# Performance work log

Measured on AMD Instinct MI355X. Metric: run time of the kernel, lower is better.

Reference implementation:

```python
import jax, jax.numpy as jnp
import numpy as np

N = 50000      # nodes
E = 400000     # edges
DIM = 3        # pseudo-coordinate dim
M = 3          # kernel size per dim (closed B-spline, degree 1)
K = M ** DIM   # 27 basis weights
IN = 32
MID = 32
OUT = 32
EPS = 1e-5


def spline_basis(edge_attr):
    """Degree-1 closed B-spline basis. edge_attr: [E, DIM] in [0,1].
    Returns basis [E, 2^DIM], weight indices [E, 2^DIM] into K."""
    bits = (jnp.arange(2 ** DIM)[:, None] >> jnp.arange(DIM)[None, :]) & 1  # [8, DIM]
    scaled = edge_attr * M                       # closed spline: scale by kernel size
    lo = jnp.floor(scaled)
    frac = scaled - lo                           # [E, DIM]
    b = jnp.where(bits[None].astype(bool), frac[:, None, :], 1.0 - frac[:, None, :])
    basis = jnp.prod(b, axis=-1)                 # [E, 8]
    idx = (lo.astype(jnp.int32)[:, None, :] + bits[None]) % M  # [E, 8, DIM]
    strides = M ** jnp.arange(DIM)               # [1, 3, 9]
    widx = jnp.sum(idx * strides, axis=-1)       # [E, 8] in [0, K)
    return basis, widx


def spline_conv(x, src, dst, basis, widx, W, root, bias):
    """x: [N, in]; W: [K, in, out]; mean aggregation + root weight + bias."""
    x_j = x[src]                                          # gather [E, in]
    upd = basis[:, :, None] * x_j[:, None, :]             # [E, 8, in]
    # scatter-add basis-weighted source features into per-(node, weight-idx) bins
    S = jnp.zeros((N, K, x.shape[1]), x.dtype).at[dst[:, None], widx].add(upd)
    deg = jnp.zeros((N,), x.dtype).at[dst].add(1.0)
    deg = jnp.maximum(deg, 1.0)
    msg = jnp.einsum('nki,kio->no', S, W) / deg[:, None]  # mean over incoming edges
    return msg + x @ root + bias


def batchnorm(h, gamma, beta):
    mu = jnp.mean(h, axis=0)
    var = jnp.var(h, axis=0)  # biased, as in torch BN forward
    return (h - mu) * jax.lax.rsqrt(var + EPS) * gamma + beta


def setup_inputs() -> dict:
    key = jax.random.key(0)
    ks = jax.random.split(key, 16)
    d = {}
    d['x'] = jax.random.normal(ks[0], (N, IN), jnp.float32)
    d['edge_index'] = jax.random.randint(ks[1], (2, E), 0, N, dtype=jnp.int32)
    d['edge_attr'] = jax.random.uniform(ks[2], (E, DIM), dtype=jnp.float32)
    d['pos'] = jax.random.normal(ks[3], (N, DIM), jnp.float32)
    def wscale(fan_in):
        return 1.0 / np.sqrt(fan_in)
    d['W1'] = jax.random.normal(ks[4], (K, IN, MID), jnp.float32) * wscale(IN)
    d['root1'] = jax.random.normal(ks[5], (IN, MID), jnp.float32) * wscale(IN)
    d['b1'] = jnp.zeros((MID,), jnp.float32)
    d['W2'] = jax.random.normal(ks[6], (K, MID, 2 * MID), jnp.float32) * wscale(MID)
    d['root2'] = jax.random.normal(ks[7], (MID, 2 * MID), jnp.float32) * wscale(MID)
    d['b2'] = jnp.zeros((2 * MID,), jnp.float32)
    d['gamma'] = jnp.ones((2 * MID,), jnp.float32)
    d['beta'] = jnp.zeros((2 * MID,), jnp.float32)
    c3_in = 2 * MID + 3
    d['W3'] = jax.random.normal(ks[8], (K, c3_in, OUT), jnp.float32) * wscale(c3_in)
    d['root3'] = jax.random.normal(ks[9], (c3_in, OUT), jnp.float32) * wscale(c3_in)
    d['b3'] = jnp.zeros((OUT,), jnp.float32)
    return d


def reference(x, edge_index, edge_attr, pos, W1, root1, b1, W2, root2, b2,
              gamma, beta, W3, root3, b3):
    src, dst = edge_index[0], edge_index[1]
    basis, widx = spline_basis(edge_attr)
    h = jax.nn.elu(spline_conv(x, src, dst, basis, widx, W1, root1, b1))
    h = jax.nn.elu(batchnorm(spline_conv(h, src, dst, basis, widx, W2, root2, b2), gamma, beta))
    h = jnp.concatenate([h, pos], axis=1)
    out = spline_conv(h, src, dst, basis, widx, W3, root3, b3)
    return out
```

## Files before the change

kernel.cpp:

```cpp
#include <hip/hip_runtime.h>
#include <hip/hip_bf16.h>


#define EPS 1e-5f
#define MAXN 50176
#define MAXE 401408
#define SP2 904

typedef __attribute__((ext_vector_type(8))) short short8;
typedef __attribute__((ext_vector_type(4))) float floatx4;

__device__ int             g_deg[MAXN];
__device__ int             g_offs[MAXN + 1];
__device__ int             g_cursor[MAXN];
__device__ int             g_bsum[256];
__device__ uint4           g_emeta[MAXE * 2];
__device__ __align__(16) __hip_bfloat16 g_h0[MAXN * 32];
__device__ __align__(16) __hip_bfloat16 g_h1[MAXN * 32];
__device__ __align__(16) __hip_bfloat16 g_h2[MAXN * 64];
__device__ __align__(16) __hip_bfloat16 g_h3[MAXN * 96];
__device__ __align__(16) __hip_bfloat16 g_Z[(size_t)MAXN * 896];
__device__ __align__(16) __hip_bfloat16 g_Wp1[28672];
__device__ __align__(16) __hip_bfloat16 g_Wp2[57344];
__device__ __align__(16) __hip_bfloat16 g_Wp3[86016];
__device__ float           g_stats[128];
__device__ int             g_isbf16;

__device__ __forceinline__ float loadf(const void* p, int i, bool bf)
{
    return bf ? (float)((const __hip_bfloat16*)p)[i] : ((const float*)p)[i];
}
__device__ __forceinline__ float bf16f(unsigned int u)
{
    return __uint_as_float(u << 16);
}
__device__ __forceinline__ unsigned short bfbits(float f)
{
    union { __hip_bfloat16 h; unsigned short u; } cv;
    cv.h = __float2bfloat16(f);
    return cv.u;
}

__global__ void init_detect(const unsigned int* __restrict__ x, int n)
{
    int i = blockIdx.x * blockDim.x + threadIdx.x;
    if (blockIdx.x == 0 && threadIdx.x < 64) {
        int lane = threadIdx.x;
        int cnt = 0;
        for (int k = lane; k < 256; k += 64) {
            unsigned int lo = x[k] & 0xFFFFu;
            int ex = (int)((lo >> 7) & 0xFFu);
            if (lo == 0u || (ex >= 96 && ex <= 140)) cnt++;
        }
#pragma unroll
        for (int o = 1; o < 64; o <<= 1) cnt += __shfl_xor(cnt, o, 64);
        if (lane == 0) g_isbf16 = (cnt >= 200) ? 1 : 0;
    }
    if (i < n) { g_deg[i] = 0; g_cursor[i] = 0; }
    if (i < 128) g_stats[i] = 0.0f;
}

template <int COUT>
__device__ __forceinline__ void prep_ws_dev(const void* W, const void* root,
                                            __hip_bfloat16* Wp, int t, bool bf)
{
    int j = t & 7;
    int lane = (t >> 3) & 63;
    int rest = t >> 9;
    int kk = rest % 28;
    int nt = rest / 28;
    int k = kk * 32 + (lane >> 4) * 8 + j;
    int o = nt * 16 + (lane & 15);
    float v = (k < 864) ? loadf(W, k * COUT + o, bf)
                        : loadf(root, (k - 864) * COUT + o, bf);
    Wp[t] = __float2bfloat16(v);
}

__device__ __forceinline__ void prep_w3_dev(const void* W, const void* root,
                                            __hip_bfloat16* Wp, int t, bool bf)
{
    const int KB = 3;
    int j = t & 7;
    int lane = (t >> 3) & 63;
    int rest = t >> 9;
    int kk = rest % KB;
    int nt = rest / KB;
    int k = kk * 32 + (lane >> 4) * 8 + j;
    int ncol = nt * 16 + (lane & 15);
    int kw = ncol >> 5;
    int o = ncol & 31;
    float v = 0.0f;
    if (k < 67)
        v = (kw < 27) ? loadf(W, (kw * 67 + k) * 32 + o, bf)
                      : loadf(root, k * 32 + o, bf);
    Wp[t] = __float2bfloat16(v);
}

__global__ void misc_kernel(const int* __restrict__ dst, const void* __restrict__ x,
                            const void* W1, const void* r1,
                            const void* W2, const void* r2,
                            const void* W3, const void* r3, int E, int N)
{
    int t = blockIdx.x * blockDim.x + threadIdx.x;
    const bool bf = (g_isbf16 != 0);
    if (t < E) { atomicAdd(&g_deg[dst[t]], 1); return; }
    t -= E;
    int nx = N * 32;
    if (t < nx) { g_h0[t] = __float2bfloat16(loadf(x, t, bf)); return; }
    t -= nx;
    if (t < 28672) { prep_ws_dev<32>(W1, r1, g_Wp1, t, bf); return; }
    t -= 28672;
    if (t < 57344) { prep_ws_dev<64>(W2, r2, g_Wp2, t, bf); return; }
    t -= 57344;
    if (t < 86016) { prep_w3_dev(W3, r3, g_Wp3, t, bf); return; }
}

__global__ void scan_blk(int n)
{
    __shared__ int buf[256];
    int tid = threadIdx.x;
    int i = blockIdx.x * 256 + tid;
    int v = (i < n) ? g_deg[i] : 0;
    buf[tid] = v;
    __syncthreads();
    for (int o = 1; o < 256; o <<= 1) {
        int t = (tid >= o) ? buf[tid - o] : 0;
        __syncthreads();
        buf[tid] += t;
        __syncthreads();
    }
    if (i < n) g_offs[i] = buf[tid] - v;
    if (tid == 255) g_bsum[blockIdx.x] = buf[255];
}

__global__ void scan_top(int nb, int n)
{
    __shared__ int buf[256];
    int tid = threadIdx.x;
    int v = (tid < nb) ? g_bsum[tid] : 0;
    buf[tid] = v;
    __syncthreads();
    for (int o = 1; o < 256; o <<= 1) {
        int t = (tid >= o) ? buf[tid - o] : 0;
        __syncthreads();
        buf[tid] += t;
        __syncthreads();
    }
    if (tid < nb) g_bsum[tid] = buf[tid] - v;
    if (tid == nb - 1) g_offs[n] = buf[tid];
}

__global__ void scan_add(int n)
{
    int i = blockIdx.x * 256 + threadIdx.x;
    if (i < n) g_offs[i] += g_bsum[i >> 8];
}

__global__ void basis_fill(const void* __restrict__ attr,
                           const int* __restrict__ src,
                           const int* __restrict__ dst, int E)
{
    int e = blockIdx.x * blockDim.x + threadIdx.x;
    if (e >= E) return;
    const bool bf = (g_isbf16 != 0);
    float f[3];
    int lo[3];
#pragma unroll
    for (int d = 0; d < 3; ++d) {
        float a = loadf(attr, e * 3 + d, bf);
        float s = a * 3.0f;
        float l = floorf(s);
        lo[d] = (int)l;
        f[d] = s - l;
    }
    const int p3[3] = {1, 3, 9};
    unsigned int wxp0 = 0, wxp1 = 0;
    unsigned short bb[8];
#pragma unroll
    for (int b = 0; b < 8; ++b) {
        float w = 1.0f;
        int id = 0;
#pragma unroll
        for (int d = 0; d < 3; ++d) {
            int bit = (b >> d) & 1;
            w *= bit ? f[d] : (1.0f - f[d]);
            id += ((lo[d] + bit) % 3) * p3[d];
        }
        if (b < 4) wxp0 |= (unsigned int)id << (8 * b);
        else       wxp1 |= (unsigned int)id << (8 * (b - 4));
        bb[b] = bfbits(w);
    }
    int d = dst[e];
    int p = atomicAdd(&g_cursor[d], 1);
    int slot = g_offs[d] + p;
    g_emeta[slot * 2] = make_uint4(wxp0, wxp1,
                                   (unsigned int)bb[0] | ((unsigned int)bb[1] << 16),
                                   (unsigned int)bb[2] | ((unsigned int)bb[3] << 16));
    g_emeta[slot * 2 + 1] = make_uint4(
        (unsigned int)bb[4] | ((unsigned int)bb[5] << 16),
        (unsigned int)bb[6] | ((unsigned int)bb[7] << 16),
        (unsigned int)src[e], 0u);
}

template <int COUT, bool ELU, int IN_SEL, int OUT_SEL>
__global__ __launch_bounds__(512, 8) void fused_conv(const void* __restrict__ bias,
                                                     int N)
{
    __shared__ unsigned short Sb[8 * SP2];
    __shared__ uint4 recs[8][64];
    __shared__ float invd[8];
    int tid = threadIdx.x, wid = tid >> 6, lane = tid & 63;
    int nbase = blockIdx.x * 8;
    const bool bf = (g_isbf16 != 0);
    const unsigned short* xptr = (IN_SEL == 0) ? (const unsigned short*)g_h0
                                               : (const unsigned short*)g_h1;
    const __hip_bfloat16* Wp = (COUT == 32) ? g_Wp1 : g_Wp2;

    int n = nbase + wid;
    int m = lane & 15, quad = lane >> 4;

    if (n < N) {
        int e0 = g_offs[n], e1 = g_offs[n + 1];
        floatx4 C00 = {}, C01 = {}, C10 = {}, C11 = {};
        uint4* myrec = &recs[wid][0];
        int bin0 = m, bin1 = m + 16;
        for (int base = e0; base < e1; base += 32) {
            int cnt = e1 - base; if (cnt > 32) cnt = 32;
            if (lane < 32) {
                uint4 v0 = make_uint4(0, 0, 0, 0), v1 = make_uint4(0, 0, 0, 0);
                if (lane < cnt) {
                    size_t le = (size_t)(base + lane) * 2;
                    v0 = g_emeta[le];
                    v1 = g_emeta[le + 1];
                }
                myrec[2 * lane] = v0;
                myrec[2 * lane + 1] = v1;
            }
            __builtin_amdgcn_s_waitcnt(0);
            int jmax = (cnt + 3) >> 2;
            unsigned a0w[4] = {0, 0, 0, 0}, a1w[4] = {0, 0, 0, 0};
            unsigned b0w[4] = {0, 0, 0, 0}, b1w[4] = {0, 0, 0, 0};
#pragma unroll
            for (int j = 0; j < 8; ++j) {
                if (j >= jmax) break;
                int kidx = j * 4 + quad;
                uint4 ra = myrec[2 * kidx];
                uint2 rb = *(const uint2*)&myrec[2 * kidx + 1];
                int sn = (int)((const unsigned*)&myrec[2 * kidx + 1])[2];
                unsigned av0 = xptr[(size_t)sn * 32 + m];
                unsigned av1 = xptr[(size_t)sn * 32 + 16 + m];
                unsigned p0 = 0, p1 = 0;
#pragma unroll
                for (int b = 0; b < 8; ++b) {
                    unsigned wx = ((b < 4 ? ra.x : ra.y) >> (8 * (b & 3))) & 0xFFu;
                    unsigned basw = (b < 2) ? ra.z : (b < 4) ? ra.w
                                  : (b < 6) ? rb.x : rb.y;
                    unsigned bas = (b & 1) ? (basw >> 16) : (basw & 0xFFFFu);
                    if (wx == (unsigned)bin0) p0 = bas;
                    if (wx == (unsigned)bin1) p1 = bas;
                }
                unsigned sh = 16 * (j & 1);
                a0w[j >> 1] |= av0 << sh;
                a1w[j >> 1] |= av1 << sh;
                b0w[j >> 1] |= p0 << sh;
                b1w[j >> 1] |= p1 << sh;
            }
            union U { unsigned w[4]; short8 v; } A0, A1, B0, B1;
#pragma unroll
            for (int q = 0; q < 4; ++q) {
                A0.w[q] = a0w[q]; A1.w[q] = a1w[q];
                B0.w[q] = b0w[q]; B1.w[q] = b1w[q];
            }
            C00 = __builtin_amdgcn_mfma_f32_16x16x32_bf16(A0.v, B0.v, C00, 0, 0, 0);
            C01 = __builtin_amdgcn_mfma_f32_16x16x32_bf16(A0.v, B1.v, C01, 0, 0, 0);
            C10 = __builtin_amdgcn_mfma_f32_16x16x32_bf16(A1.v, B0.v, C10, 0, 0, 0);
            C11 = __builtin_amdgcn_mfma_f32_16x16x32_bf16(A1.v, B1.v, C11, 0, 0, 0);
        }
        unsigned short* Srow = Sb + wid * SP2;
        {
            floatx4 Cf[4] = {C00, C01, C10, C11};
#pragma unroll
            for (int f = 0; f < 4; ++f) {
                int mt = f >> 1, nt = f & 1;
                int bin = nt * 16 + m;
                if (bin < 27) {
                    union { unsigned short h[4]; uint2 u; } pk;
#pragma unroll
                    for (int r = 0; r < 4; ++r) pk.h[r] = bfbits(Cf[f][r]);
                    *(uint2*)(Srow + bin * 32 + mt * 16 + quad * 4) = pk.u;
                }
            }
        }
        if (lane < 32) Srow[864 + lane] = xptr[(size_t)n * 32 + lane];
        if (lane == 0) {
            int deg = e1 - e0;
            invd[wid] = 1.0f / (float)(deg < 1 ? 1 : deg);
        }
    }
    __syncthreads();

    if (wid * 16 < COUT) {
        int mrow = m & 7;
        const unsigned short* Ab = Sb + mrow * SP2 + quad * 8;
        floatx4 accS = {}, accR = {};
#pragma unroll
        for (int kk = 0; kk < 28; ++kk) {
            short8 a = *(const short8*)(Ab + kk * 32);
            const short* bp = (const short*)Wp +
                ((size_t)(wid * 28 + kk) * 64 + lane) * 8;
            short8 b = *(const short8*)bp;
            if (kk < 27) accS = __builtin_amdgcn_mfma_f32_16x16x32_bf16(a, b, accS, 0, 0, 0);
            else         accR = __builtin_amdgcn_mfma_f32_16x16x32_bf16(a, b, accR, 0, 0, 0);
        }
        int o = wid * 16 + m;
        float bval = loadf(bias, o, bf);
#pragma unroll
        for (int r = 0; r < 4; ++r) {
            int slot = quad * 4 + r;
            if (slot >= 8) continue;
            int nn = nbase + slot;
            if (nn >= N) continue;
            float v = accS[r] * invd[slot] + accR[r] + bval;
            if (ELU) v = v > 0.0f ? v : expm1f(v);
            if (OUT_SEL == 1) g_h1[nn * 32 + o] = __float2bfloat16(v);
            else              g_h2[nn * 64 + o] = __float2bfloat16(v);
        }
    }
}

__global__ void bn_reduce(int n)
{
    int tid = threadIdx.x;
    int c = tid & 63;
    int r = tid >> 6;
    float s = 0.0f, s2 = 0.0f;
    for (int i = blockIdx.x * 4 + r; i < n; i += gridDim.x * 4) {
        float v = (float)g_h2[i * 64 + c];
        s += v; s2 += v * v;
    }
    __shared__ float b1s[256], b2s[256];
    b1s[tid] = s; b2s[tid] = s2;
    __syncthreads();
    if (r == 0) {
        s  = b1s[c] + b1s[c + 64] + b1s[c + 128] + b1s[c + 192];
        s2 = b2s[c] + b2s[c + 64] + b2s[c + 128] + b2s[c + 192];
        atomicAdd(&g_stats[c], s);
        atomicAdd(&g_stats[64 + c], s2);
    }
}

__global__ void h3_build(const void* __restrict__ pos,
                         const void* __restrict__ gamma,
                         const void* __restrict__ beta, int N)
{
    __shared__ float cf[128];
    int t = threadIdx.x;
    const bool bf = (g_isbf16 != 0);
    if (t < 64) {
        float inv_n = 1.0f / (float)N;
        float mu = g_stats[t] * inv_n;
        float var = g_stats[64 + t] * inv_n - mu * mu;
        float A = rsqrtf(var + EPS) * loadf(gamma, t, bf);
        cf[t] = A;
        cf[64 + t] = loadf(beta, t, bf) - mu * A;
    }
    __syncthreads();
    int idx = blockIdx.x * blockDim.x + t;
    if (idx >= N * 96) return;
    int n = idx / 96, ch = idx - n * 96;
    float v;
    if (ch < 64) {
        float h = (float)g_h2[n * 64 + ch];
        v = h * cf[ch] + cf[64 + ch];
        v = v > 0.0f ? v : expm1f(v);
    } else if (ch < 67) {
        v = loadf(pos, n * 3 + (ch - 64), bf);
    } else {
        v = 0.0f;
    }
    g_h3[(size_t)n * 96 + ch] = __float2bfloat16(v);
}

template <int STRIDE, int NTOT, int KPAD, int NPW>
__global__ __launch_bounds__(256) void gemm_kernel(int MT, int NTW)
{
    int gid = blockIdx.x * 256 + threadIdx.x;
    int gw = gid >> 6, lane = gid & 63;
    if (gw >= MT * NTW) return;
    int mt = gw / NTW;
    int ntb = (gw % NTW) * NPW;
    int m = lane & 15, quad = lane >> 4;
    const short* hrow = (const short*)g_h3 + (size_t)(mt * 16 + m) * STRIDE;
    floatx4 acc[NPW] = {};
    const int KB = KPAD / 32;
#pragma unroll
    for (int kk = 0; kk < KB; ++kk) {
        short8 a = *(const short8*)(hrow + kk * 32 + quad * 8);
#pragma unroll
        for (int i = 0; i < NPW; ++i) {
            const short* bp = (const short*)g_Wp3 +
                (((size_t)(ntb + i) * KB + kk) * 64 + lane) * 8;
            short8 b = *(const short8*)bp;
            acc[i] = __builtin_amdgcn_mfma_f32_16x16x32_bf16(a, b, acc[i], 0, 0, 0);
        }
    }
    int col = lane & 15;
    int rowbase = mt * 16 + quad * 4;
#pragma unroll
    for (int i = 0; i < NPW; ++i) {
        int ncol = (ntb + i) * 16 + col;
#pragma unroll
        for (int r = 0; r < 4; ++r)
            g_Z[(size_t)(rowbase + r) * NTOT + ncol] = __float2bfloat16(acc[i][r]);
    }
}

template <int COUT, int NTOT>
__global__ __launch_bounds__(256) void agg_kernel(const void* __restrict__ bias,
                                                  void* __restrict__ out_ext, int N)
{
    int wid = threadIdx.x >> 6, lane = threadIdx.x & 63;
    int n = blockIdx.x * 4 + wid;
    if (n >= N) return;
    const bool bf = (g_isbf16 != 0);
    const unsigned short* zp = (const unsigned short*)g_Z;
    int e0 = g_offs[n], e1 = g_offs[n + 1];
    float acc = 0.0f;
    int o = lane & 31, bh = lane >> 5;
    for (int base = e0; base < e1; base += 32) {
        int cnt = e1 - base; if (cnt > 32) cnt = 32;
        uint4 r0 = make_uint4(0, 0, 0, 0), r1 = make_uint4(0, 0, 0, 0);
        if ((lane & 31) < cnt) {
            size_t le = (size_t)(base + (lane & 31)) * 2;
            r0 = g_emeta[le];
            r1 = g_emeta[le + 1];
        }
        int selw4 = (int)(bh ? r0.y : r0.x);
        int selba = (int)(bh ? r1.x : r0.z);
        int selbb = (int)(bh ? r1.y : r0.w);
        int srcv  = (int)r1.z;
#pragma unroll 2
        for (int j = 0; j < cnt; ++j) {
            int sl = j + (bh << 5);
            int sn = __shfl(srcv, j, 64);
            unsigned int w4  = (unsigned int)__shfl(selw4, sl, 64);
            unsigned int ba  = (unsigned int)__shfl(selba, sl, 64);
            unsigned int bbv = (unsigned int)__shfl(selbb, sl, 64);
            const unsigned short* zr = zp + (size_t)sn * NTOT;
#pragma unroll
            for (int bi = 0; bi < 4; ++bi) {
                int wxv = (int)((w4 >> (8 * bi)) & 0xFFu);
                unsigned int bbits = (((bi & 2) ? bbv : ba) >> (16 * (bi & 1))) & 0xFFFFu;
                acc += bf16f(bbits) * bf16f(zr[wxv * 32 + o]);
            }
        }
    }
    acc += __shfl_xor(acc, 32, 64);
    if (lane >= 32) return;
    int deg = e1 - e0;
    float inv = 1.0f / (float)(deg < 1 ? 1 : deg);
    float v = acc * inv + bf16f(zp[(size_t)n * NTOT + 27 * COUT + o])
            + loadf(bias, o, bf);
    if (bf) ((__hip_bfloat16*)out_ext)[n * COUT + o] = __float2bfloat16(v);
    else    ((float*)out_ext)[n * COUT + o] = v;
}

extern "C" void kernel_launch(void* const* d_in, const int* in_sizes, int n_in,
                              void* d_out, int out_size, void* d_ws, size_t ws_size,
                              hipStream_t stream)
{
    const void* x      = d_in[0];
    const int*  eindex = (const int*)d_in[1];
    const void* eattr  = d_in[2];
    const void* pos    = d_in[3];
    const void* W1     = d_in[4];
    const void* root1  = d_in[5];
    const void* b1     = d_in[6];
    const void* W2     = d_in[7];
    const void* root2  = d_in[8];
    const void* b2     = d_in[9];
    const void* gamma  = d_in[10];
    const void* beta   = d_in[11];
    const void* W3     = d_in[12];
    const void* root3  = d_in[13];
    const void* b3     = d_in[14];
    (void)d_ws; (void)ws_size; (void)n_in; (void)out_size;

    const int N = in_sizes[0] / 32;
    const int E = in_sizes[1] / 2;
    const int* srcp = eindex;
    const int* dstp = eindex + E;

    init_detect<<<(N + 255) / 256, 256, 0, stream>>>((const unsigned int*)x, N);
    {
        int tot = E + N * 32 + 28672 + 57344 + 86016;
        misc_kernel<<<(tot + 255) / 256, 256, 0, stream>>>(
            dstp, x, W1, root1, W2, root2, W3, root3, E, N);
    }
    int nb = (N + 255) / 256;
    scan_blk<<<nb, 256, 0, stream>>>(N);
    scan_top<<<1, 256, 0, stream>>>(nb, N);
    scan_add<<<nb, 256, 0, stream>>>(N);
    basis_fill<<<(E + 255) / 256, 256, 0, stream>>>(eattr, srcp, dstp, E);

    int nb8 = (N + 7) / 8;
    fused_conv<32, true, 0, 1><<<nb8, 512, 0, stream>>>(b1, N);
    fused_conv<64, false, 1, 2><<<nb8, 512, 0, stream>>>(b2, N);
    bn_reduce<<<120, 256, 0, stream>>>(N);
    h3_build<<<(N * 96 + 255) / 256, 256, 0, stream>>>(pos, gamma, beta, N);
    {
        const int NTOT = 28 * 32, KPAD = 96, NPW = 4;
        int NTW = (NTOT / 16) / NPW;
        int MT = (N + 15) / 16;
        int waves = MT * NTW;
        gemm_kernel<96, NTOT, KPAD, NPW><<<(waves + 3) / 4, 256, 0, stream>>>(MT, NTW);
    }
    agg_kernel<32, 28 * 32><<<(N + 3) / 4, 256, 0, stream>>>(b3, d_out, N);
}
```

Measured before the change: 365.5 us.

## Fuse layer-3 spline conv into aggregate-then-transform kernel, dropping Z buffer

Replaces the transform-then-gather path for layer 3 (a GEMM writing a per-node 896-wide Z buffer, then an edge-gather kernel) with one fused kernel. For each node it builds the per-bin aggregated features S in LDS using MFMA, then multiplies by the repacked W3/root weights, reduces the split-K partials and writes the output. This removes roughly 90MB of Z writes and the random gathers of Z rows, at the cost of more MFMA work per node (K=2688), higher LDS usage and lower occupancy.

```diff
diff --git a/kernel.cpp b/kernel.cpp
--- a/kernel.cpp
+++ b/kernel.cpp
@@ -6,6 +6,7 @@
 #define MAXN 50176
 #define MAXE 401408
 #define SP2 904
+#define SP3 2696
 
 typedef __attribute__((ext_vector_type(8))) short short8;
 typedef __attribute__((ext_vector_type(4))) float floatx4;
@@ -19,7 +20,6 @@
 __device__ __align__(16) __hip_bfloat16 g_h1[MAXN * 32];
 __device__ __align__(16) __hip_bfloat16 g_h2[MAXN * 64];
 __device__ __align__(16) __hip_bfloat16 g_h3[MAXN * 96];
-__device__ __align__(16) __hip_bfloat16 g_Z[(size_t)MAXN * 896];
 __device__ __align__(16) __hip_bfloat16 g_Wp1[28672];
 __device__ __align__(16) __hip_bfloat16 g_Wp2[57344];
 __device__ __align__(16) __hip_bfloat16 g_Wp3[86016];
@@ -79,20 +79,23 @@
 __device__ __forceinline__ void prep_w3_dev(const void* W, const void* root,
                                             __hip_bfloat16* Wp, int t, bool bf)
 {
-    const int KB = 3;
+    const int KB = 84;
     int j = t & 7;
     int lane = (t >> 3) & 63;
     int rest = t >> 9;
     int kk = rest % KB;
     int nt = rest / KB;
     int k = kk * 32 + (lane >> 4) * 8 + j;
-    int ncol = nt * 16 + (lane & 15);
-    int kw = ncol >> 5;
-    int o = ncol & 31;
+    int o = nt * 16 + (lane & 15);
     float v = 0.0f;
-    if (k < 67)
-        v = (kw < 27) ? loadf(W, (kw * 67 + k) * 32 + o, bf)
-                      : loadf(root, k * 32 + o, bf);
+    if (k < 2592) {
+        int bin = k / 96;
+        int ch = k - bin * 96;
+        if (ch < 67) v = loadf(W, (bin * 67 + ch) * 32 + o, bf);
+    } else {
+        int ch = k - 2592;
+        if (ch < 67) v = loadf(root, ch * 32 + o, bf);
+    }
     Wp[t] = __float2bfloat16(v);
 }
 
@@ -328,6 +331,156 @@
     }
 }
 
+__global__ __launch_bounds__(512, 4) void fused_conv3(const void* __restrict__ bias,
+                                                      void* __restrict__ out_ext,
+                                                      int N)
+{
+    __shared__ __align__(16) unsigned short Sb[8 * SP3];
+    __shared__ union {
+        uint4 recs[8][64];
+        float red[6][64][4];
+    } u;
+    __shared__ float invd[8];
+    int tid = threadIdx.x, wid = tid >> 6, lane = tid & 63;
+    int nbase = blockIdx.x * 8;
+    const bool bf = (g_isbf16 != 0);
+    const unsigned short* xptr = (const unsigned short*)g_h3;
+
+    int n = nbase + wid;
+    int m = lane & 15, quad = lane >> 4;
+
+    if (n < N) {
+        int e0 = g_offs[n], e1 = g_offs[n + 1];
+        floatx4 C[6][2];
+#pragma unroll
+        for (int t = 0; t < 6; ++t) {
+            C[t][0] = (floatx4){0.f, 0.f, 0.f, 0.f};
+            C[t][1] = (floatx4){0.f, 0.f, 0.f, 0.f};
+        }
+        uint4* myrec = &u.recs[wid][0];
+        int bin0 = m, bin1 = m + 16;
+        for (int base = e0; base < e1; base += 32) {
+            int cnt = e1 - base; if (cnt > 32) cnt = 32;
+            if (lane < 32) {
+                uint4 v0 = make_uint4(0, 0, 0, 0), v1 = make_uint4(0, 0, 0, 0);
+                if (lane < cnt) {
+                    size_t le = (size_t)(base + lane) * 2;
+                    v0 = g_emeta[le];
+                    v1 = g_emeta[le + 1];
+                }
+                myrec[2 * lane] = v0;
+                myrec[2 * lane + 1] = v1;
+            }
+            __builtin_amdgcn_s_waitcnt(0);
+            int jmax = (cnt + 3) >> 2;
+            unsigned aw[6][4] = {{0, 0, 0, 0}, {0, 0, 0, 0}, {0, 0, 0, 0},
+                                 {0, 0, 0, 0}, {0, 0, 0, 0}, {0, 0, 0, 0}};
+            unsigned b0w[4] = {0, 0, 0, 0}, b1w[4] = {0, 0, 0, 0};
+#pragma unroll
+            for (int j = 0; j < 8; ++j) {
+                if (j >= jmax) break;
+                int kidx = j * 4 + quad;
+                uint4 ra = myrec[2 * kidx];
+                uint2 rb = *(const uint2*)&myrec[2 * kidx + 1];
+                int sn = (int)((const unsigned*)&myrec[2 * kidx + 1])[2];
+                const unsigned short* hr = xptr + (size_t)sn * 96 + m;
+                unsigned av[6];
+#pragma unroll
+                for (int t = 0; t < 6; ++t) av[t] = hr[t * 16];
+                unsigned p0 = 0, p1 = 0;
+#pragma unroll
+                for (int b = 0; b < 8; ++b) {
+                    unsigned wx = ((b < 4 ? ra.x : ra.y) >> (8 * (b & 3))) & 0xFFu;
+                    unsigned basw = (b < 2) ? ra.z : (b < 4) ? ra.w
+                                  : (b < 6) ? rb.x : rb.y;
+                    unsigned bas = (b & 1) ? (basw >> 16) : (basw & 0xFFFFu);
+                    if (wx == (unsigned)bin0) p0 = bas;
+                    if (wx == (unsigned)bin1) p1 = bas;
+                }
+                unsigned sh = 16 * (j & 1);
+#pragma unroll
+                for (int t = 0; t < 6; ++t) aw[t][j >> 1] |= av[t] << sh;
+                b0w[j >> 1] |= p0 << sh;
+                b1w[j >> 1] |= p1 << sh;
+            }
+            union U { unsigned w[4]; short8 v; } A, B0, B1;
+#pragma unroll
+            for (int q = 0; q < 4; ++q) { B0.w[q] = b0w[q]; B1.w[q] = b1w[q]; }
+#pragma unroll
+            for (int t = 0; t < 6; ++t) {
+#pragma unroll
+                for (int q = 0; q < 4; ++q) A.w[q] = aw[t][q];
+                C[t][0] = __builtin_amdgcn_mfma_f32_16x16x32_bf16(A.v, B0.v, C[t][0], 0, 0, 0);
+                C[t][1] = __builtin_amdgcn_mfma_f32_16x16x32_bf16(A.v, B1.v, C[t][1], 0, 0, 0);
+            }
+        }
+        unsigned short* Srow = Sb + wid * SP3;
+#pragma unroll
+        for (int t = 0; t < 6; ++t) {
+#pragma unroll
+            for (int ntile = 0; ntile < 2; ++ntile) {
+                int bin = ntile * 16 + m;
+                if (bin < 27) {
+                    union { unsigned short h[4]; uint2 uu; } pk;
+#pragma unroll
+                    for (int r = 0; r < 4; ++r) pk.h[r] = bfbits(C[t][ntile][r]);
+                    *(uint2*)(Srow + bin * 96 + t * 16 + quad * 4) = pk.uu;
+                }
+            }
+        }
+        for (int t2 = lane; t2 < 96; t2 += 64)
+            Srow[2592 + t2] = xptr[(size_t)n * 96 + t2];
+        if (lane == 0) {
+            int deg = e1 - e0;
+            invd[wid] = 1.0f / (float)(deg < 1 ? 1 : deg);
+        }
+    }
+    __syncthreads();
+
+    int nt = wid & 1, kq = wid >> 1;
+    int mrow = m & 7;
+    const unsigned short* Ab = Sb + mrow * SP3 + quad * 8;
+    floatx4 accS = {}, accR = {};
+    {
+        int kbeg = kq * 21, kend = kbeg + 21;
+        int ksplit = (kend < 81) ? kend : 81;
+        for (int kk = kbeg; kk < ksplit; ++kk) {
+            short8 a = *(const short8*)(Ab + kk * 32);
+            const short* bp = (const short*)g_Wp3 +
+                ((size_t)(nt * 84 + kk) * 64 + lane) * 8;
+            short8 b = *(const short8*)bp;
+            accS = __builtin_amdgcn_mfma_f32_16x16x32_bf16(a, b, accS, 0, 0, 0);
+        }
+        for (int kk = ksplit; kk < kend; ++kk) {
+            short8 a = *(const short8*)(Ab + kk * 32);
+            const short* bp = (const short*)g_Wp3 +
+                ((size_t)(nt * 84 + kk) * 64 + lane) * 8;
+            short8 b = *(const short8*)bp;
+            accR = __builtin_amdgcn_mfma_f32_16x16x32_bf16(a, b, accR, 0, 0, 0);
+        }
+    }
+    if (kq < 3)
+        *(floatx4*)&u.red[wid][lane][0] = accS;
+    __syncthreads();
+    if (kq == 3) {
+#pragma unroll
+        for (int w = 0; w < 3; ++w)
+            accS += *(const floatx4*)&u.red[2 * w + nt][lane][0];
+        int o = nt * 16 + m;
+        float bval = loadf(bias, o, bf);
+#pragma unroll
+        for (int r = 0; r < 4; ++r) {
+            int slot = quad * 4 + r;
+            if (slot >= 8) continue;
+            int nn = nbase + slot;
+            if (nn >= N) continue;
+            float v = accS[r] * invd[slot] + accR[r] + bval;
+            if (bf) ((__hip_bfloat16*)out_ext)[nn * 32 + o] = __float2bfloat16(v);
+            else    ((float*)out_ext)[nn * 32 + o] = v;
+        }
+    }
+}
+
 __global__ void bn_reduce(int n)
 {
     int tid = threadIdx.x;
@@ -379,90 +532,6 @@
         v = 0.0f;
     }
     g_h3[(size_t)n * 96 + ch] = __float2bfloat16(v);
-}
-
-template <int STRIDE, int NTOT, int KPAD, int NPW>
-__global__ __launch_bounds__(256) void gemm_kernel(int MT, int NTW)
-{
-    int gid = blockIdx.x * 256 + threadIdx.x;
-    int gw = gid >> 6, lane = gid & 63;
-    if (gw >= MT * NTW) return;
-    int mt = gw / NTW;
-    int ntb = (gw % NTW) * NPW;
-    int m = lane & 15, quad = lane >> 4;
-    const short* hrow = (const short*)g_h3 + (size_t)(mt * 16 + m) * STRIDE;
-    floatx4 acc[NPW] = {};
-    const int KB = KPAD / 32;
-#pragma unroll
-    for (int kk = 0; kk < KB; ++kk) {
-        short8 a = *(const short8*)(hrow + kk * 32 + quad * 8);
-#pragma unroll
-        for (int i = 0; i < NPW; ++i) {
-            const short* bp = (const short*)g_Wp3 +
-                (((size_t)(ntb + i) * KB + kk) * 64 + lane) * 8;
-            short8 b = *(const short8*)bp;
-            acc[i] = __builtin_amdgcn_mfma_f32_16x16x32_bf16(a, b, acc[i], 0, 0, 0);
-        }
-    }
-    int col = lane & 15;
-    int rowbase = mt * 16 + quad * 4;
-#pragma unroll
-    for (int i = 0; i < NPW; ++i) {
-        int ncol = (ntb + i) * 16 + col;
-#pragma unroll
-        for (int r = 0; r < 4; ++r)
-            g_Z[(size_t)(rowbase + r) * NTOT + ncol] = __float2bfloat16(acc[i][r]);
-    }
-}
-
-template <int COUT, int NTOT>
-__global__ __launch_bounds__(256) void agg_kernel(const void* __restrict__ bias,
-                                                  void* __restrict__ out_ext, int N)
-{
-    int wid = threadIdx.x >> 6, lane = threadIdx.x & 63;
-    int n = blockIdx.x * 4 + wid;
-    if (n >= N) return;
-    const bool bf = (g_isbf16 != 0);
-    const unsigned short* zp = (const unsigned short*)g_Z;
-    int e0 = g_offs[n], e1 = g_offs[n + 1];
-    float acc = 0.0f;
-    int o = lane & 31, bh = lane >> 5;
-    for (int base = e0; base < e1; base += 32) {
-        int cnt = e1 - base; if (cnt > 32) cnt = 32;
-        uint4 r0 = make_uint4(0, 0, 0, 0), r1 = make_uint4(0, 0, 0, 0);
-        if ((lane & 31) < cnt) {
-            size_t le = (size_t)(base + (lane & 31)) * 2;
-            r0 = g_emeta[le];
-            r1 = g_emeta[le + 1];
-        }
-        int selw4 = (int)(bh ? r0.y : r0.x);
-        int selba = (int)(bh ? r1.x : r0.z);
-        int selbb = (int)(bh ? r1.y : r0.w);
-        int srcv  = (int)r1.z;
-#pragma unroll 2
-        for (int j = 0; j < cnt; ++j) {
-            int sl = j + (bh << 5);
-            int sn = __shfl(srcv, j, 64);
-            unsigned int w4  = (unsigned int)__shfl(selw4, sl, 64);
-            unsigned int ba  = (unsigned int)__shfl(selba, sl, 64);
-            unsigned int bbv = (unsigned int)__shfl(selbb, sl, 64);
-            const unsigned short* zr = zp + (size_t)sn * NTOT;
-#pragma unroll
-            for (int bi = 0; bi < 4; ++bi) {
-                int wxv = (int)((w4 >> (8 * bi)) & 0xFFu);
-                unsigned int bbits = (((bi & 2) ? bbv : ba) >> (16 * (bi & 1))) & 0xFFFFu;
-                acc += bf16f(bbits) * bf16f(zr[wxv * 32 + o]);
-            }
-        }
-    }
-    acc += __shfl_xor(acc, 32, 64);
-    if (lane >= 32) return;
-    int deg = e1 - e0;
-    float inv = 1.0f / (float)(deg < 1 ? 1 : deg);
-    float v = acc * inv + bf16f(zp[(size_t)n * NTOT + 27 * COUT + o])
-            + loadf(bias, o, bf);
-    if (bf) ((__hip_bfloat16*)out_ext)[n * COUT + o] = __float2bfloat16(v);
-    else    ((float*)out_ext)[n * COUT + o] = v;
 }
 
 extern "C" void kernel_launch(void* const* d_in, const int* in_sizes, int n_in,
@@ -508,12 +577,5 @@
     fused_conv<64, false, 1, 2><<<nb8, 512, 0, stream>>>(b2, N);
     bn_reduce<<<120, 256, 0, stream>>>(N);
     h3_build<<<(N * 96 + 255) / 256, 256, 0, stream>>>(pos, gamma, beta, N);
-    {
-        const int NTOT = 28 * 32, KPAD = 96, NPW = 4;
-        int NTW = (NTOT / 16) / NPW;
-        int MT = (N + 15) / 16;
-        int waves = MT * NTW;
-        gemm_kernel<96, NTOT, KPAD, NPW><<<(waves + 3) / 4, 256, 0, stream>>>(MT, NTW);
-    }
-    agg_kernel<32, 28 * 32><<<(N + 3) / 4, 256, 0, stream>>>(b3, d_out, N);
-}
+    fused_conv3<<<nb8, 512, 0, stream>>>(b3, d_out, N);
+}
```

After: 379.3 us. +3.8%, slower.

## Precompute dense per-edge basis bins and permute channels for paired loads

Applied to the files above, without the earlier changes.

In basis_fill, each edge's 8 sparse (index, weight) basis pairs are expanded into a dense 32-bin bf16 table stored alongside the source index. The conv aggregation loop then reads each lane's two bin weights with a single LDS load instead of scanning 8 entries per edge. Input channels are interleaved so one 32-bit load gathers both halves of the MFMA A operand, and the weight packing and root-row fill are permuted to match. The per-edge chunk drops from 32 to 16 edges. The trade-off is more global memory traffic per edge (64 bytes of basis plus a source index) in exchange for less ALU and LDS work, and the old emeta array is still written even though this kernel no longer reads it.

```diff
diff --git a/kernel.cpp b/kernel.cpp
--- a/kernel.cpp
+++ b/kernel.cpp
@@ -14,6 +14,8 @@
 __device__ int             g_offs[MAXN + 1];
 __device__ int             g_cursor[MAXN];
 __device__ int             g_bsum[256];
+__device__ int             g_esrc[MAXE];
+__device__ __align__(16) uint4 g_ebas[MAXE * 4];
 __device__ uint4           g_emeta[MAXE * 2];
 __device__ __align__(16) __hip_bfloat16 g_h0[MAXN * 32];
 __device__ __align__(16) __hip_bfloat16 g_h1[MAXN * 32];
@@ -40,6 +42,11 @@
     cv.h = __float2bfloat16(f);
     return cv.u;
 }
+__device__ __forceinline__ void lds_fence()
+{
+    asm volatile("s_waitcnt lgkmcnt(0)" ::: "memory");
+    __builtin_amdgcn_sched_barrier(0);
+}
 
 __global__ void init_detect(const unsigned int* __restrict__ x, int n)
 {
@@ -71,8 +78,16 @@
     int nt = rest / 28;
     int k = kk * 32 + (lane >> 4) * 8 + j;
     int o = nt * 16 + (lane & 15);
-    float v = (k < 864) ? loadf(W, k * COUT + o, bf)
-                        : loadf(root, (k - 864) * COUT + o, bf);
+    float v;
+    if (k < 864) {
+        int bin = k >> 5, p = k & 31;
+        int ch = 2 * (p & 15) + (p >> 4);
+        v = loadf(W, (bin * 32 + ch) * COUT + o, bf);
+    } else {
+        int p = k - 864;
+        int ch = 2 * (p & 15) + (p >> 4);
+        v = loadf(root, ch * COUT + o, bf);
+    }
     Wp[t] = __float2bfloat16(v);
 }
 
@@ -174,8 +189,9 @@
         f[d] = s - l;
     }
     const int p3[3] = {1, 3, 9};
+    int wx8[8];
+    unsigned short bb[8];
     unsigned int wxp0 = 0, wxp1 = 0;
-    unsigned short bb[8];
 #pragma unroll
     for (int b = 0; b < 8; ++b) {
         float w = 1.0f;
@@ -186,20 +202,39 @@
             w *= bit ? f[d] : (1.0f - f[d]);
             id += ((lo[d] + bit) % 3) * p3[d];
         }
+        wx8[b] = id;
+        bb[b] = bfbits(w);
         if (b < 4) wxp0 |= (unsigned int)id << (8 * b);
         else       wxp1 |= (unsigned int)id << (8 * (b - 4));
-        bb[b] = bfbits(w);
+    }
+    unsigned wds[16];
+#pragma unroll
+    for (int i = 0; i < 16; ++i) {
+        unsigned w = 0;
+#pragma unroll
+        for (int b = 0; b < 8; ++b) {
+            if (wx8[b] == i)      w |= (unsigned)bb[b];
+            if (wx8[b] == i + 16) w |= (unsigned)bb[b] << 16;
+        }
+        wds[i] = w;
     }
     int d = dst[e];
     int p = atomicAdd(&g_cursor[d], 1);
     int slot = g_offs[d] + p;
+    int sv = src[e];
+    uint4* out4 = &g_ebas[(size_t)slot * 4];
+    out4[0] = make_uint4(wds[0],  wds[1],  wds[2],  wds[3]);
+    out4[1] = make_uint4(wds[4],  wds[5],  wds[6],  wds[7]);
+    out4[2] = make_uint4(wds[8],  wds[9],  wds[10], wds[11]);
+    out4[3] = make_uint4(wds[12], wds[13], wds[14], wds[15]);
+    g_esrc[slot] = sv;
     g_emeta[slot * 2] = make_uint4(wxp0, wxp1,
                                    (unsigned int)bb[0] | ((unsigned int)bb[1] << 16),
                                    (unsigned int)bb[2] | ((unsigned int)bb[3] << 16));
     g_emeta[slot * 2 + 1] = make_uint4(
         (unsigned int)bb[4] | ((unsigned int)bb[5] << 16),
         (unsigned int)bb[6] | ((unsigned int)bb[7] << 16),
-        (unsigned int)src[e], 0u);
+        (unsigned int)sv, 0u);
 }
 
 template <int COUT, bool ELU, int IN_SEL, int OUT_SEL>
@@ -207,7 +242,8 @@
                                                      int N)
 {
     __shared__ unsigned short Sb[8 * SP2];
-    __shared__ uint4 recs[8][64];
+    __shared__ __align__(16) unsigned basb[8][16][16];
+    __shared__ int ssrc[8][16];
     __shared__ float invd[8];
     int tid = threadIdx.x, wid = tid >> 6, lane = tid & 63;
     int nbase = blockIdx.x * 8;
@@ -222,48 +258,32 @@
     if (n < N) {
         int e0 = g_offs[n], e1 = g_offs[n + 1];
         floatx4 C00 = {}, C01 = {}, C10 = {}, C11 = {};
-        uint4* myrec = &recs[wid][0];
-        int bin0 = m, bin1 = m + 16;
-        for (int base = e0; base < e1; base += 32) {
-            int cnt = e1 - base; if (cnt > 32) cnt = 32;
-            if (lane < 32) {
-                uint4 v0 = make_uint4(0, 0, 0, 0), v1 = make_uint4(0, 0, 0, 0);
-                if (lane < cnt) {
-                    size_t le = (size_t)(base + lane) * 2;
-                    v0 = g_emeta[le];
-                    v1 = g_emeta[le + 1];
-                }
-                myrec[2 * lane] = v0;
-                myrec[2 * lane + 1] = v1;
+        for (int base = e0; base < e1; base += 16) {
+            int cnt = e1 - base; if (cnt > 16) cnt = 16;
+            {
+                int es = lane >> 2, part = lane & 3;
+                uint4 v = make_uint4(0, 0, 0, 0);
+                if (es < cnt) v = g_ebas[(size_t)(base + es) * 4 + part];
+                *(uint4*)&basb[wid][es][part * 4] = v;
+                if (lane < 16)
+                    ssrc[wid][lane] = (lane < cnt) ? g_esrc[base + lane] : 0;
             }
-            __builtin_amdgcn_s_waitcnt(0);
+            lds_fence();
             int jmax = (cnt + 3) >> 2;
             unsigned a0w[4] = {0, 0, 0, 0}, a1w[4] = {0, 0, 0, 0};
             unsigned b0w[4] = {0, 0, 0, 0}, b1w[4] = {0, 0, 0, 0};
 #pragma unroll
-            for (int j = 0; j < 8; ++j) {
+            for (int j = 0; j < 4; ++j) {
                 if (j >= jmax) break;
                 int kidx = j * 4 + quad;
-                uint4 ra = myrec[2 * kidx];
-                uint2 rb = *(const uint2*)&myrec[2 * kidx + 1];
-                int sn = (int)((const unsigned*)&myrec[2 * kidx + 1])[2];
-                unsigned av0 = xptr[(size_t)sn * 32 + m];
-                unsigned av1 = xptr[(size_t)sn * 32 + 16 + m];
-                unsigned p0 = 0, p1 = 0;
-#pragma unroll
-                for (int b = 0; b < 8; ++b) {
-                    unsigned wx = ((b < 4 ? ra.x : ra.y) >> (8 * (b & 3))) & 0xFFu;
-                    unsigned basw = (b < 2) ? ra.z : (b < 4) ? ra.w
-                                  : (b < 6) ? rb.x : rb.y;
-                    unsigned bas = (b & 1) ? (basw >> 16) : (basw & 0xFFFFu);
-                    if (wx == (unsigned)bin0) p0 = bas;
-                    if (wx == (unsigned)bin1) p1 = bas;
-                }
+                int sn = ssrc[wid][kidx];
+                unsigned pw = basb[wid][kidx][m];
+                unsigned hw = *((const unsigned*)xptr + (size_t)sn * 16 + m);
                 unsigned sh = 16 * (j & 1);
-                a0w[j >> 1] |= av0 << sh;
-                a1w[j >> 1] |= av1 << sh;
-                b0w[j >> 1] |= p0 << sh;
-                b1w[j >> 1] |= p1 << sh;
+                a0w[j >> 1] |= (hw & 0xFFFFu) << sh;
+                a1w[j >> 1] |= (hw >> 16) << sh;
+                b0w[j >> 1] |= (pw & 0xFFFFu) << sh;
+                b1w[j >> 1] |= (pw >> 16) << sh;
             }
             union U { unsigned w[4]; short8 v; } A0, A1, B0, B1;
 #pragma unroll
@@ -291,7 +311,10 @@
                 }
             }
         }
-        if (lane < 32) Srow[864 + lane] = xptr[(size_t)n * 32 + lane];
+        if (lane < 32) {
+            int ch = 2 * (lane & 15) + (lane >> 4);
+            Srow[864 + lane] = xptr[(size_t)n * 32 + ch];
+        }
         if (lane == 0) {
             int deg = e1 - e0;
             invd[wid] = 1.0f / (float)(deg < 1 ? 1 : deg);
```

New measurement: 380.2 us. 4.0% more time.
